# Optimization experiments

Measured on AMD Instinct MI355X. Metric: run time of the kernel, lower is better.

## Reference

```python
import jax, jax.numpy as jnp
import numpy as np

P = 2.0            # power-mean exponent (init kwarg p)
NUM_NODES = 1_000_000
D_FEAT = 128
NUM_GRAPHS = 4096


def setup_inputs() -> dict:
    key = jax.random.key(0)
    kx, kb = jax.random.split(key)
    x = jax.random.normal(kx, (NUM_NODES, D_FEAT), dtype=jnp.float32)
    batch = jnp.sort(jax.random.randint(kb, (NUM_NODES,), 0, NUM_GRAPHS, dtype=jnp.int64))
    return {"x": x, "batch": batch}


def reference(x, batch):
    # x: [N, D] node features; batch: [N] sorted graph ids in [0, NUM_GRAPHS)
    xp = x ** P                                                   # elementwise pow
    seg_sum = jax.ops.segment_sum(xp, batch, num_segments=NUM_GRAPHS)  # [G, D]
    counts = jax.ops.segment_sum(jnp.ones((x.shape[0],), dtype=x.dtype), batch,
                                 num_segments=NUM_GRAPHS)         # [G]
    # scatter_mean semantics: empty segments yield 0 (clamp count to avoid 0/0)
    mean = seg_sum / jnp.maximum(counts, 1.0)[:, None]            # [G, D]
    return mean ** (1.0 / P)
```

## Files before the change

kernel.cpp:

```cpp
#include <hip/hip_runtime.h>
#include <math.h>


#define D_FEAT 128
#define DV (D_FEAT / 4)

__global__ __launch_bounds__(256) void global_powermean_pooling_44126493999223_kernel(
    const float* __restrict__ x,
    const int* __restrict__ batch,
    float* __restrict__ out,
    int N)
{
    const int g    = blockIdx.x;
    const int tid  = threadIdx.x;
    const int fg   = tid & 31;
    const int lane = tid >> 5;

    __shared__ int s_range[2];
    if (tid < 2) {
        const int key = g + tid;
        int lo = 0, hi = N;
        while (lo < hi) {
            int mid = (lo + hi) >> 1;
            if (batch[mid] < key) lo = mid + 1; else hi = mid;
        }
        s_range[tid] = lo;
    }
    __syncthreads();
    const int start = s_range[0];
    const int end   = s_range[1];
    const int count = end - start;

    const float4* __restrict__ x4 = (const float4*)x;
    float4 acc = make_float4(0.f, 0.f, 0.f, 0.f);
    for (int r = start + lane; r < end; r += 8) {
        float4 v = x4[(size_t)r * DV + fg];
        acc.x += v.x * v.x;
        acc.y += v.y * v.y;
        acc.z += v.z * v.z;
        acc.w += v.w * v.w;
    }

    __shared__ float4 red[256];
    red[tid] = acc;
    __syncthreads();
    for (int off = 4; off >= 1; off >>= 1) {
        if (lane < off) {
            float4 a = red[tid];
            float4 b = red[tid + off * 32];
            a.x += b.x; a.y += b.y; a.z += b.z; a.w += b.w;
            red[tid] = a;
        }
        __syncthreads();
    }

    if (lane == 0) {
        const float inv = 1.0f / (float)(count > 0 ? count : 1);
        float4 s = red[tid];
        float4 o;
        o.x = sqrtf(s.x * inv);
        o.y = sqrtf(s.y * inv);
        o.z = sqrtf(s.z * inv);
        o.w = sqrtf(s.w * inv);
        ((float4*)out)[(size_t)g * DV + fg] = o;
    }
}

extern "C" void kernel_launch(void* const* d_in, const int* in_sizes, int n_in,
                              void* d_out, int out_size, void* d_ws, size_t ws_size,
                              hipStream_t stream) {
    const float* x     = (const float*)d_in[0];
    const int*   batch = (const int*)d_in[1];
    float*       out   = (float*)d_out;

    const int N = in_sizes[1];
    const int G = out_size / D_FEAT;

    global_powermean_pooling_44126493999223_kernel<<<G, 256, 0, stream>>>(x, batch, out, N);
}
```

Measured before the change: 656.9 us.

## Precompute segment offsets in a separate kernel and unroll row accumulation

Adds a pre-pass kernel that writes CSR-style segment boundaries from the sorted batch array into workspace, replacing the per-block binary search over batch. The pooling kernel also unrolls the row loop by four with independent accumulators, so more loads are in flight per thread. The cost is an extra kernel launch and a full read of the batch array. The boundary fill relies on the workspace holding at least G+1 ints.

```diff
diff --git a/kernel.cpp b/kernel.cpp
--- a/kernel.cpp
+++ b/kernel.cpp
@@ -5,49 +5,69 @@
 #define D_FEAT 128
 #define DV (D_FEAT / 4)
 
+__global__ __launch_bounds__(256) void seg_offsets_kernel(
+    const int* __restrict__ batch, int* __restrict__ off, int N, int G)
+{
+    int i = blockIdx.x * blockDim.x + threadIdx.x;
+    if (i >= N) return;
+    int cur = batch[i];
+    if (i == 0) {
+        for (int g = 0; g <= cur; ++g) off[g] = 0;
+    } else {
+        int prev = batch[i - 1];
+        for (int g = prev + 1; g <= cur; ++g) off[g] = i;
+    }
+    if (i == N - 1) {
+        for (int g = cur + 1; g <= G; ++g) off[g] = N;
+    }
+}
+
 __global__ __launch_bounds__(256) void global_powermean_pooling_44126493999223_kernel(
     const float* __restrict__ x,
-    const int* __restrict__ batch,
-    float* __restrict__ out,
-    int N)
+    const int* __restrict__ off,
+    float* __restrict__ out)
 {
     const int g    = blockIdx.x;
     const int tid  = threadIdx.x;
     const int fg   = tid & 31;
     const int lane = tid >> 5;
 
-    __shared__ int s_range[2];
-    if (tid < 2) {
-        const int key = g + tid;
-        int lo = 0, hi = N;
-        while (lo < hi) {
-            int mid = (lo + hi) >> 1;
-            if (batch[mid] < key) lo = mid + 1; else hi = mid;
-        }
-        s_range[tid] = lo;
-    }
-    __syncthreads();
-    const int start = s_range[0];
-    const int end   = s_range[1];
+    const int start = off[g];
+    const int end   = off[g + 1];
     const int count = end - start;
 
     const float4* __restrict__ x4 = (const float4*)x;
-    float4 acc = make_float4(0.f, 0.f, 0.f, 0.f);
-    for (int r = start + lane; r < end; r += 8) {
+
+    float4 a0 = make_float4(0.f, 0.f, 0.f, 0.f);
+    float4 a1 = a0, a2 = a0, a3 = a0;
+
+    int r = start + lane;
+    for (; r + 24 < end; r += 32) {
+        float4 v0 = x4[(size_t)(r     ) * DV + fg];
+        float4 v1 = x4[(size_t)(r +  8) * DV + fg];
+        float4 v2 = x4[(size_t)(r + 16) * DV + fg];
+        float4 v3 = x4[(size_t)(r + 24) * DV + fg];
+        a0.x += v0.x * v0.x; a0.y += v0.y * v0.y; a0.z += v0.z * v0.z; a0.w += v0.w * v0.w;
+        a1.x += v1.x * v1.x; a1.y += v1.y * v1.y; a1.z += v1.z * v1.z; a1.w += v1.w * v1.w;
+        a2.x += v2.x * v2.x; a2.y += v2.y * v2.y; a2.z += v2.z * v2.z; a2.w += v2.w * v2.w;
+        a3.x += v3.x * v3.x; a3.y += v3.y * v3.y; a3.z += v3.z * v3.z; a3.w += v3.w * v3.w;
+    }
+    for (; r < end; r += 8) {
         float4 v = x4[(size_t)r * DV + fg];
-        acc.x += v.x * v.x;
-        acc.y += v.y * v.y;
-        acc.z += v.z * v.z;
-        acc.w += v.w * v.w;
+        a0.x += v.x * v.x; a0.y += v.y * v.y; a0.z += v.z * v.z; a0.w += v.w * v.w;
     }
+    a0.x += a1.x + a2.x + a3.x;
+    a0.y += a1.y + a2.y + a3.y;
+    a0.z += a1.z + a2.z + a3.z;
+    a0.w += a1.w + a2.w + a3.w;
 
     __shared__ float4 red[256];
-    red[tid] = acc;
+    red[tid] = a0;
     __syncthreads();
-    for (int off = 4; off >= 1; off >>= 1) {
-        if (lane < off) {
+    for (int o = 4; o >= 1; o >>= 1) {
+        if (lane < o) {
             float4 a = red[tid];
-            float4 b = red[tid + off * 32];
+            float4 b = red[tid + o * 32];
             a.x += b.x; a.y += b.y; a.z += b.z; a.w += b.w;
             red[tid] = a;
         }
@@ -76,5 +96,8 @@
     const int N = in_sizes[1];
     const int G = out_size / D_FEAT;
 
-    global_powermean_pooling_44126493999223_kernel<<<G, 256, 0, stream>>>(x, batch, out, N);
+    int* off = (int*)d_ws;
+
+    seg_offsets_kernel<<<(N + 255) / 256, 256, 0, stream>>>(batch, off, N, G);
+    global_powermean_pooling_44126493999223_kernel<<<G, 256, 0, stream>>>(x, off, out);
 }
```

New measurement: 651.4 us. No clear change (-0.8%).
